# Optimization experiments

Measured on AMD Instinct MI355X. Metric: run time of the kernel, lower is better.

## Reference

```python
import jax, jax.numpy as jnp
from jax import lax
import numpy as np

B, CIN, H, W = 8, 3, 512, 512
BASE = 32
TOPK = 200
SCORE_T = 0.01
IOU_T = 0.5
DN = ('NCHW', 'OIHW', 'NCHW')


def setup_inputs() -> dict:
    key = jax.random.key(0)
    ks = jax.random.split(key, 12)
    def conv_w(k, o, i, kh, kw):
        fan_in = i * kh * kw
        return jax.random.normal(k, (o, i, kh, kw), jnp.float32) * (1.0 / np.sqrt(fan_in))
    c = [CIN, BASE, BASE * 2, BASE * 4, BASE * 8]
    inp = {'images': jax.random.normal(ks[0], (B, CIN, H, W), jnp.float32)}
    for l in range(4):
        inp[f'w{l+1}'] = conv_w(ks[1 + 2 * l], c[l + 1], c[l], 3, 3)
        inp[f'b{l+1}'] = jnp.zeros((c[l + 1],), jnp.float32)
    inp['wh'] = conv_w(ks[9], 5, c[4], 1, 1)
    inp['bh'] = jnp.zeros((5,), jnp.float32)
    return inp


def _conv_relu_pool(x, w, b):
    x = lax.conv_general_dilated(x, w, (1, 1), 'SAME', dimension_numbers=DN)
    x = jax.nn.relu(x + b[None, :, None, None])
    return lax.reduce_window(x, -jnp.inf, lax.max, (1, 1, 2, 2), (1, 1, 2, 2), 'VALID')


def _decode(pred):
    # pred: [B,5,Gh,Gw]
    Bn, _, Gh, Gw = pred.shape
    sy, sx = H / float(Gh), W / float(Gw)
    obj = jax.nn.sigmoid(pred[:, 0])
    tx = jax.nn.sigmoid(pred[:, 1])
    ty = jax.nn.sigmoid(pred[:, 2])
    bw = jnp.exp(pred[:, 3]) * sx
    bh = jnp.exp(pred[:, 4]) * sy
    gy = jnp.arange(Gh, dtype=pred.dtype)[None, :, None]
    gx = jnp.arange(Gw, dtype=pred.dtype)[None, None, :]
    cx = gx * sx + tx * sx
    cy = gy * sy + ty * sy
    x1 = jnp.clip(cx - bw / 2.0, 0.0, W - 1)
    y1 = jnp.clip(cy - bh / 2.0, 0.0, H - 1)
    x2 = jnp.clip(cx + bw / 2.0, 0.0, W - 1)
    y2 = jnp.clip(cy + bh / 2.0, 0.0, H - 1)
    boxes = jnp.stack([x1, y1, x2, y2], axis=-1).reshape(Bn, Gh * Gw, 4)
    scores = obj.reshape(Bn, Gh * Gw)
    # score threshold + top-k (fixed size, padded with invalid entries)
    masked = jnp.where(scores >= SCORE_T, scores, -1.0)
    svals, sidx = lax.top_k(masked, TOPK)                      # [B,K]
    boxes_k = jnp.take_along_axis(boxes, sidx[:, :, None], axis=1)  # [B,K,4]
    valid = svals >= SCORE_T
    # pairwise IoU [B,K,K]
    bx1, by1, bx2, by2 = (boxes_k[..., i] for i in range(4))
    area = (bx2 - bx1) * (by2 - by1)
    xx1 = jnp.maximum(bx1[:, :, None], bx1[:, None, :])
    yy1 = jnp.maximum(by1[:, :, None], by1[:, None, :])
    xx2 = jnp.minimum(bx2[:, :, None], bx2[:, None, :])
    yy2 = jnp.minimum(by2[:, :, None], by2[:, None, :])
    inter = jnp.clip(xx2 - xx1, 0.0) * jnp.clip(yy2 - yy1, 0.0)
    union = area[:, :, None] + area[:, None, :] - inter
    iou = inter / jnp.maximum(union, 1e-6)
    ar = jnp.arange(TOPK)
    def body(i, keep):  # greedy NMS over score-sorted boxes
        sup = (iou[:, i, :] > IOU_T) & (ar[None, :] > i) & keep[:, i][:, None]
        return keep & ~sup
    keep = lax.fori_loop(0, TOPK, body, valid)
    scores_k = jnp.where(valid, svals, 0.0)
    return boxes_k, scores_k, keep


def reference(images, w1, b1, w2, b2, w3, b3, w4, b4, wh, bh):
    x = _conv_relu_pool(images, w1, b1)
    x = _conv_relu_pool(x, w2, b2)
    x = _conv_relu_pool(x, w3, b3)
    x = _conv_relu_pool(x, w4, b4)
    pred = lax.conv_general_dilated(x, wh, (1, 1), 'SAME', dimension_numbers=DN)
    pred = pred + bh[None, :, None, None]
    boxes, scores, keep = _decode(pred)
    kf = keep.astype(boxes.dtype)
    out5 = jnp.concatenate([boxes, scores[..., None]], axis=-1) * kf[..., None]
    return out5, keep
```

## Files before the change

kernel.cpp:

```cpp
#include <hip/hip_runtime.h>
#include <math.h>


constexpr int TOPK_N = 200;

template <int CIN, int CI_BLK, int CO_BLK>
__launch_bounds__(256)
__global__ void conv_relu_pool_pipe(const float* __restrict__ in,
                                    const float* __restrict__ wgt,
                                    const float* __restrict__ bias,
                                    float* __restrict__ out,
                                    int Hin, int Win, int Cout) {
    constexpr int SPATIAL = 34 * 34;
    constexpr int SSLOT = (SPATIAL + 255) / 256;
    constexpr int NW = CI_BLK * 9 * CO_BLK;
    constexpr int NCHUNK = CIN / CI_BLK;
    const int Hp = Hin >> 1, Wp = Win >> 1;
    const int coChunks = Cout / CO_BLK;
    const int b  = blockIdx.z / coChunks;
    const int cz = blockIdx.z % coChunks;
    const int tid = threadIdx.x;
    const int tx = tid & 15, ty = tid >> 4;
    const int px = (blockIdx.x << 4) + tx;
    const int py = (blockIdx.y << 4) + ty;
    const int iy0 = (blockIdx.y << 5) - 1;
    const int ix0 = (blockIdx.x << 5) - 1;

    __shared__ float  s_in[2][CI_BLK * SPATIAL];
    __shared__ double s_w[2][NW];

    int soff[SSLOT];
#pragma unroll
    for (int s = 0; s < SSLOT; ++s) {
        const int cell = tid + s * 256;
        int g = -1;
        if (cell < SPATIAL) {
            const int ly = cell / 34, lx = cell - ly * 34;
            const int iy = iy0 + ly, ix = ix0 + lx;
            if ((unsigned)iy < (unsigned)Hin && (unsigned)ix < (unsigned)Win)
                g = iy * Win + ix;
        }
        soff[s] = g;
    }
    int wg = -1;
    if (tid < NW) {
        const int co   = tid & (CO_BLK - 1);
        const int rest = tid / CO_BLK;
        const int k    = rest % 9;
        const int ci   = rest / 9;
        wg = ((cz * CO_BLK + co) * CIN + ci) * 9 + k;
    }
    const size_t HW = (size_t)Hin * Win;
    const float* in_b = in + (size_t)b * CIN * HW;

    double acc[CO_BLK][4];
#pragma unroll
    for (int co = 0; co < CO_BLK; ++co)
#pragma unroll
        for (int p = 0; p < 4; ++p) acc[co][p] = 0.0;

    float rin[CI_BLK][SSLOT];
    float rw = 0.f;

#pragma unroll
    for (int ci = 0; ci < CI_BLK; ++ci) {
        const float* src = in_b + ci * HW;
#pragma unroll
        for (int s = 0; s < SSLOT; ++s) {
            const int cell = tid + s * 256;
            float v = 0.f;
            if (cell < SPATIAL) { const int g = soff[s]; if (g >= 0) v = src[g]; }
            rin[ci][s] = v;
        }
    }
    if (tid < NW) rw = wgt[wg];
#pragma unroll
    for (int ci = 0; ci < CI_BLK; ++ci)
#pragma unroll
        for (int s = 0; s < SSLOT; ++s) {
            const int cell = tid + s * 256;
            if (cell < SPATIAL) s_in[0][ci * SPATIAL + cell] = rin[ci][s];
        }
    if (tid < NW) s_w[0][tid] = (double)rw;
    __syncthreads();

    for (int c = 0; c < NCHUNK; ++c) {
        const int buf = c & 1;
        if (c + 1 < NCHUNK) {
            const int c0n = (c + 1) * CI_BLK;
#pragma unroll
            for (int ci = 0; ci < CI_BLK; ++ci) {
                const float* src = in_b + (c0n + ci) * HW;
#pragma unroll
                for (int s = 0; s < SSLOT; ++s) {
                    const int cell = tid + s * 256;
                    float v = 0.f;
                    if (cell < SPATIAL) { const int g = soff[s]; if (g >= 0) v = src[g]; }
                    rin[ci][s] = v;
                }
            }
            if (tid < NW) rw = wgt[wg + c0n * 9];
        }
#pragma unroll 1
        for (int ci = 0; ci < CI_BLK; ++ci) {
            const float* tile = &s_in[buf][ci * SPATIAL];
            double win[4][4];
#pragma unroll
            for (int iy = 0; iy < 4; ++iy) {
                float2 r0 = *(const float2*)&tile[(2 * ty + iy) * 34 + 2 * tx];
                float2 r1 = *(const float2*)&tile[(2 * ty + iy) * 34 + 2 * tx + 2];
                win[iy][0] = (double)r0.x; win[iy][1] = (double)r0.y;
                win[iy][2] = (double)r1.x; win[iy][3] = (double)r1.y;
            }
#pragma unroll
            for (int k = 0; k < 9; ++k) {
                const int ky = k / 3, kx = k % 3;
                const double* wp = &s_w[buf][(ci * 9 + k) * CO_BLK];
                double w[CO_BLK];
#pragma unroll
                for (int co = 0; co < CO_BLK; ++co) w[co] = wp[co];
#pragma unroll
                for (int p = 0; p < 4; ++p) {
                    const double v = win[(p >> 1) + ky][(p & 1) + kx];
#pragma unroll
                    for (int co = 0; co < CO_BLK; ++co)
                        acc[co][p] = fma(v, w[co], acc[co][p]);
                }
            }
        }
        if (c + 1 < NCHUNK) {
#pragma unroll
            for (int ci = 0; ci < CI_BLK; ++ci)
#pragma unroll
                for (int s = 0; s < SSLOT; ++s) {
                    const int cell = tid + s * 256;
                    if (cell < SPATIAL) s_in[buf ^ 1][ci * SPATIAL + cell] = rin[ci][s];
                }
            if (tid < NW) s_w[buf ^ 1][tid] = (double)rw;
            __syncthreads();
        }
    }

#pragma unroll
    for (int co = 0; co < CO_BLK; ++co) {
        const double bd = (double)bias[cz * CO_BLK + co];
        const float e0 = fmaxf((float)(acc[co][0] + bd), 0.f);
        const float e1 = fmaxf((float)(acc[co][1] + bd), 0.f);
        const float e2 = fmaxf((float)(acc[co][2] + bd), 0.f);
        const float e3 = fmaxf((float)(acc[co][3] + bd), 0.f);
        out[((size_t)(b * Cout + cz * CO_BLK + co) * Hp + py) * Wp + px] =
            fmaxf(fmaxf(e0, e1), fmaxf(e2, e3));
    }
}

__launch_bounds__(256)
__global__ void head_decode_k(const float* __restrict__ x4,
                              const float* __restrict__ wh,
                              const float* __restrict__ bh,
                              float* __restrict__ boxes,
                              float* __restrict__ scores) {
    __shared__ float s_wh[5 * 256];
    const int tid = threadIdx.x;
#pragma unroll
    for (int i = 0; i < 5; ++i) s_wh[i * 256 + tid] = wh[i * 256 + tid];
    __syncthreads();

    const int idx  = blockIdx.x * 256 + tid;
    const int b    = idx >> 10;
    const int cell = idx & 1023;
    const int gy = cell >> 5, gx = cell & 31;

    double a0 = (double)bh[0], a1 = (double)bh[1], a2 = (double)bh[2],
           a3 = (double)bh[3], a4 = (double)bh[4];
    const float* xp = x4 + b * 262144 + cell;
    for (int ci = 0; ci < 256; ++ci) {
        const double v = (double)xp[ci << 10];
        a0 = fma(v, (double)s_wh[0 * 256 + ci], a0);
        a1 = fma(v, (double)s_wh[1 * 256 + ci], a1);
        a2 = fma(v, (double)s_wh[2 * 256 + ci], a2);
        a3 = fma(v, (double)s_wh[3 * 256 + ci], a3);
        a4 = fma(v, (double)s_wh[4 * 256 + ci], a4);
    }
    const double obj = 1.0 / (1.0 + exp(-a0));
    const double txs = 1.0 / (1.0 + exp(-a1));
    const double tys = 1.0 / (1.0 + exp(-a2));
    const double bw  = exp(a3) * 16.0;
    const double bhh = exp(a4) * 16.0;
    const double cx  = gx * 16.0 + txs * 16.0;
    const double cy  = gy * 16.0 + tys * 16.0;
    float* bp = boxes + idx * 4;
    bp[0] = (float)fmin(fmax(cx - bw * 0.5, 0.0), 511.0);
    bp[1] = (float)fmin(fmax(cy - bhh * 0.5, 0.0), 511.0);
    bp[2] = (float)fmin(fmax(cx + bw * 0.5, 0.0), 511.0);
    bp[3] = (float)fmin(fmax(cy + bhh * 0.5, 0.0), 511.0);
    scores[idx] = (float)obj;
}

__launch_bounds__(256)
__global__ void topk_nms_k(const float* __restrict__ boxes,
                           const float* __restrict__ scores,
                           float* __restrict__ out5,
                           float* __restrict__ keep_out) {
    const int b = blockIdx.x, tid = threadIdx.x;
    __shared__ unsigned long long key[1024];
    __shared__ float bx1[TOPK_N], by1[TOPK_N], bx2[TOPK_N], by2[TOPK_N];
    __shared__ float sv[TOPK_N], ar[TOPK_N];
    __shared__ int   kp[TOPK_N];

    for (int i = tid; i < 1024; i += 256) {
        float s = scores[b * 1024 + i];
        float m = (s >= 0.01f) ? s : -1.0f;
        unsigned u = __float_as_uint(m);
        u = (u & 0x80000000u) ? ~u : (u | 0x80000000u);
        key[i] = ((unsigned long long)u << 32) | (unsigned)(1023 - i);
    }
    __syncthreads();

    for (int k = 2; k <= 1024; k <<= 1) {
        for (int j = k >> 1; j > 0; j >>= 1) {
            for (int i = tid; i < 1024; i += 256) {
                int l = i ^ j;
                if (l > i) {
                    unsigned long long a = key[i], c = key[l];
                    bool desc = ((i & k) == 0);
                    bool sw = desc ? (a < c) : (a > c);
                    if (sw) { key[i] = c; key[l] = a; }
                }
            }
            __syncthreads();
        }
    }

    for (int i = tid; i < TOPK_N; i += 256) {
        unsigned long long kk = key[i];
        unsigned u = (unsigned)(kk >> 32);
        unsigned bits = (u & 0x80000000u) ? (u & 0x7FFFFFFFu) : ~u;
        float s = __uint_as_float(bits);
        int src = 1023 - (int)(kk & 0xFFFFFFFFu);
        const float4 bb = *(const float4*)(boxes + (b * 1024 + src) * 4);
        bx1[i] = bb.x; by1[i] = bb.y; bx2[i] = bb.z; by2[i] = bb.w;
        sv[i] = s;
        ar[i] = (bb.z - bb.x) * (bb.w - bb.y);
        kp[i] = (s >= 0.01f) ? 1 : 0;
    }
    __syncthreads();

    for (int i = 0; i < TOPK_N; ++i) {
        if (kp[i]) {
            const float X1 = bx1[i], Y1 = by1[i], X2 = bx2[i], Y2 = by2[i], A = ar[i];
            for (int j = tid; j < TOPK_N; j += 256) {
                if (j > i && kp[j]) {
                    float xx1 = fmaxf(X1, bx1[j]);
                    float yy1 = fmaxf(Y1, by1[j]);
                    float xx2 = fminf(X2, bx2[j]);
                    float yy2 = fminf(Y2, by2[j]);
                    float inter = fmaxf(xx2 - xx1, 0.f) * fmaxf(yy2 - yy1, 0.f);
                    float uni = A + ar[j] - inter;
                    float iou = inter / fmaxf(uni, 1e-6f);
                    if (iou > 0.5f) kp[j] = 0;
                }
            }
        }
        __syncthreads();
    }

    for (int i = tid; i < TOPK_N; i += 256) {
        float kf = kp[i] ? 1.f : 0.f;
        float s  = sv[i];
        float sc = (s >= 0.01f) ? s : 0.f;
        float* op = out5 + (b * TOPK_N + i) * 5;
        op[0] = bx1[i] * kf;
        op[1] = by1[i] * kf;
        op[2] = bx2[i] * kf;
        op[3] = by2[i] * kf;
        op[4] = sc * kf;
        keep_out[b * TOPK_N + i] = kf;
    }
}

extern "C" void kernel_launch(void* const* d_in, const int* in_sizes, int n_in,
                              void* d_out, int out_size, void* d_ws, size_t ws_size,
                              hipStream_t stream) {
    const float* images = (const float*)d_in[0];
    const float* w1 = (const float*)d_in[1];
    const float* b1 = (const float*)d_in[2];
    const float* w2 = (const float*)d_in[3];
    const float* b2 = (const float*)d_in[4];
    const float* w3 = (const float*)d_in[5];
    const float* b3 = (const float*)d_in[6];
    const float* w4 = (const float*)d_in[7];
    const float* b4 = (const float*)d_in[8];
    const float* wh = (const float*)d_in[9];
    const float* bh = (const float*)d_in[10];
    float* out = (float*)d_out;

    float* A    = (float*)d_ws;
    float* Bbuf = A + 16777216;
    float* boxes  = A + 8388608;
    float* scores = A + 8388608 + 32768;

    conv_relu_pool_pipe<3, 3, 8><<<dim3(16, 16, 8 * 4), 256, 0, stream>>>(
        images, w1, b1, A, 512, 512, 32);
    conv_relu_pool_pipe<32, 2, 8><<<dim3(8, 8, 8 * 8), 256, 0, stream>>>(
        A, w2, b2, Bbuf, 256, 256, 64);
    conv_relu_pool_pipe<64, 2, 8><<<dim3(4, 4, 8 * 16), 256, 0, stream>>>(
        Bbuf, w3, b3, A, 128, 128, 128);
    conv_relu_pool_pipe<128, 2, 8><<<dim3(2, 2, 8 * 32), 256, 0, stream>>>(
        A, w4, b4, Bbuf, 64, 64, 256);
    head_decode_k<<<32, 256, 0, stream>>>(Bbuf, wh, bh, boxes, scores);
    topk_nms_k<<<8, 256, 0, stream>>>(boxes, scores, out, out + 8 * TOPK_N * 5);
}
```

Measured before the change: 1.341 ms.

## Run conv layers 2-4 on FP64 MFMA with a runtime layout probe

```diff
diff --git a/kernel.cpp b/kernel.cpp
--- a/kernel.cpp
+++ b/kernel.cpp
@@ -3,6 +3,166 @@
 
 
 constexpr int TOPK_N = 200;
+
+typedef double f64x4 __attribute__((ext_vector_type(4)));
+
+__launch_bounds__(64)
+__global__ void mfma_probe_k(int* flag) {
+    const int l = threadIdx.x;
+    const int lm = l & 15, z = l >> 4;
+    const double af = 1.0 + (double)l;
+    const double bf = 2.0 + (double)(l * l);
+    f64x4 acc = {0.0, 0.0, 0.0, 0.0};
+    acc = __builtin_amdgcn_mfma_f64_16x16x4f64(af, bf, acc, 0, 0, 0);
+
+    int found = -1;
+    for (int Ci = 0; Ci < 4; ++Ci)
+        for (int Ai = 0; Ai < 2; ++Ai)
+            for (int Bi = 0; Bi < 2; ++Bi) {
+                bool ok = true;
+                for (int r = 0; r < 4; ++r) {
+                    int m, n;
+                    if (Ci == 0)      { m = 4 * z + r; n = lm; }
+                    else if (Ci == 1) { m = lm;        n = 4 * z + r; }
+                    else if (Ci == 2) { m = z + 4 * r; n = lm; }
+                    else              { m = lm;        n = z + 4 * r; }
+                    double e = 0.0;
+                    for (int k = 0; k < 4; ++k) {
+                        const int la = Ai ? (4 * m + k) : (m + 16 * k);
+                        const int lb = Bi ? (4 * n + k) : (16 * k + n);
+                        e += (1.0 + (double)la) * (2.0 + (double)(lb * lb));
+                    }
+                    if (fabs(acc[r] - e) > 0.5) { ok = false; break; }
+                }
+                const unsigned long long vote = __ballot(ok);
+                if (vote == ~0ULL && found < 0) found = Ci * 4 + Ai * 2 + Bi;
+            }
+    if (l == 0) *flag = found;
+}
+
+template <int CIN>
+__launch_bounds__(256)
+__global__ void conv_mfma(const float* __restrict__ in,
+                          const float* __restrict__ wgt,
+                          const float* __restrict__ bias,
+                          float* __restrict__ out,
+                          const int* __restrict__ flag_p,
+                          int Hin, int Win, int Cout) {
+    const int Hp = Hin >> 1, Wp = Win >> 1;
+    const int coChunks = Cout >> 4;
+    const int b  = blockIdx.z / coChunks;
+    const int cz = blockIdx.z % coChunks;
+    const int tid = threadIdx.x;
+    const int lane = tid & 63;
+    const int wv = tid >> 6;
+    const int lm = lane & 15, z = lane >> 4;
+
+    int combo = flag_p[0];
+    if (combo < 0 || combo > 15) combo = 0;
+    const int Ci = combo >> 2, Ai = (combo >> 1) & 1, Bi = combo & 1;
+
+    const int ma = Ai ? (lane >> 2) : lm;
+    const int ka = Ai ? (lane & 3) : z;
+    const int kb = Bi ? (lane & 3) : z;
+    const int nb = Bi ? (lane >> 2) : lm;
+
+    __shared__ double s_halo[4 * 324];
+    __shared__ double s_wB[576];
+    __shared__ float  s_pool[4][4][16][16];
+
+    int off[9];
+#pragma unroll
+    for (int j = 0; j < 9; ++j) {
+        const int t = 4 * j + ka;
+        const int ciL = t / 9, k = t - ciL * 9;
+        const int ky = k / 3, kx = k - ky * 3;
+        off[j] = ciL * 324 + ky * 18 + kx;
+    }
+    int baseT[4];
+    {
+        const int s = ma & 3, dy = s >> 1, dx = s & 1, r = ma >> 2;
+#pragma unroll
+        for (int T = 0; T < 4; ++T) {
+            const int p = wv * 16 + T * 4 + r;
+            const int ey = 2 * (p >> 3) + dy, ex = 2 * (p & 7) + dx;
+            baseT[T] = ey * 18 + ex;
+        }
+    }
+
+    const size_t HW = (size_t)Hin * Win;
+    const float* in_b = in + (size_t)b * CIN * HW;
+    const int gy0 = blockIdx.y * 16, gx0 = blockIdx.x * 16;
+
+    f64x4 acc[4];
+#pragma unroll
+    for (int T = 0; T < 4; ++T) acc[T] = (f64x4){0.0, 0.0, 0.0, 0.0};
+
+    for (int c0 = 0; c0 < CIN; c0 += 4) {
+        __syncthreads();
+        for (int s = 0; s < 6; ++s) {
+            const int idx = tid + s * 256;
+            if (idx < 1296) {
+                const int ciL = idx / 324;
+                const int rem = idx - ciL * 324;
+                const int hy = rem / 18, hx = rem - hy * 18;
+                const int iy = gy0 - 1 + hy, ix = gx0 - 1 + hx;
+                double v = 0.0;
+                if ((unsigned)iy < (unsigned)Hin && (unsigned)ix < (unsigned)Win)
+                    v = (double)in_b[(size_t)(c0 + ciL) * HW + iy * Win + ix];
+                s_halo[idx] = v;
+            }
+        }
+        for (int s = 0; s < 3; ++s) {
+            const int e = tid + s * 256;
+            if (e < 576) {
+                const int co = e & 15, t = e >> 4;
+                const int ciL = t / 9, k = t - ciL * 9;
+                s_wB[e] = (double)wgt[((cz * 16 + co) * CIN + c0 + ciL) * 9 + k];
+            }
+        }
+        __syncthreads();
+
+#pragma unroll
+        for (int j = 0; j < 9; ++j) {
+            const double bf = s_wB[(4 * j + kb) * 16 + nb];
+#pragma unroll
+            for (int T = 0; T < 4; ++T) {
+                const double af = s_halo[baseT[T] + off[j]];
+                acc[T] = __builtin_amdgcn_mfma_f64_16x16x4f64(af, bf, acc[T], 0, 0, 0);
+            }
+        }
+    }
+
+    __syncthreads();
+#pragma unroll
+    for (int T = 0; T < 4; ++T) {
+#pragma unroll
+        for (int r = 0; r < 4; ++r) {
+            int m, n;
+            if (Ci == 0)      { m = 4 * z + r; n = lm; }
+            else if (Ci == 1) { m = lm;        n = 4 * z + r; }
+            else if (Ci == 2) { m = z + 4 * r; n = lm; }
+            else              { m = lm;        n = z + 4 * r; }
+            const float v =
+                fmaxf((float)(acc[T][r] + (double)bias[cz * 16 + n]), 0.f);
+            s_pool[wv][T][m][n] = v;
+        }
+    }
+    __syncthreads();
+    for (int e = tid; e < 1024; e += 256) {
+        const int n  = e & 15;
+        const int pr = e >> 4;
+        const int wvv = pr >> 4, Tr = (pr >> 2) & 3, r = pr & 3;
+        const float v0 = s_pool[wvv][Tr][4 * r + 0][n];
+        const float v1 = s_pool[wvv][Tr][4 * r + 1][n];
+        const float v2 = s_pool[wvv][Tr][4 * r + 2][n];
+        const float v3 = s_pool[wvv][Tr][4 * r + 3][n];
+        const float mx = fmaxf(fmaxf(v0, v1), fmaxf(v2, v3));
+        const int py = blockIdx.y * 8 + (pr >> 3);
+        const int px = blockIdx.x * 8 + (pr & 7);
+        out[((size_t)(b * Cout + cz * 16 + n) * Hp + py) * Wp + px] = mx;
+    }
+}
 
 template <int CIN, int CI_BLK, int CO_BLK>
 __launch_bounds__(256)
@@ -298,15 +458,17 @@
     float* Bbuf = A + 16777216;
     float* boxes  = A + 8388608;
     float* scores = A + 8388608 + 32768;
-
+    int*   flag   = (int*)d_out;
+
+    mfma_probe_k<<<1, 64, 0, stream>>>(flag);
     conv_relu_pool_pipe<3, 3, 8><<<dim3(16, 16, 8 * 4), 256, 0, stream>>>(
         images, w1, b1, A, 512, 512, 32);
-    conv_relu_pool_pipe<32, 2, 8><<<dim3(8, 8, 8 * 8), 256, 0, stream>>>(
-        A, w2, b2, Bbuf, 256, 256, 64);
-    conv_relu_pool_pipe<64, 2, 8><<<dim3(4, 4, 8 * 16), 256, 0, stream>>>(
-        Bbuf, w3, b3, A, 128, 128, 128);
-    conv_relu_pool_pipe<128, 2, 8><<<dim3(2, 2, 8 * 32), 256, 0, stream>>>(
-        A, w4, b4, Bbuf, 64, 64, 256);
+    conv_mfma<32><<<dim3(16, 16, 8 * 4), 256, 0, stream>>>(
+        A, w2, b2, Bbuf, flag, 256, 256, 64);
+    conv_mfma<64><<<dim3(8, 8, 8 * 8), 256, 0, stream>>>(
+        Bbuf, w3, b3, A, flag, 128, 128, 128);
+    conv_mfma<128><<<dim3(4, 4, 8 * 16), 256, 0, stream>>>(
+        A, w4, b4, Bbuf, flag, 64, 64, 256);
     head_decode_k<<<32, 256, 0, stream>>>(Bbuf, wh, bh, boxes, scores);
     topk_nms_k<<<8, 256, 0, stream>>>(boxes, scores, out, out + 8 * TOPK_N * 5);
 }
```

New measurement: 1.414 ms. +5.4%, slower.
